# Performance work log

Measured on AMD Instinct MI355X. Metric: run time of the kernel, lower is better.

Reference implementation:

```python
import jax, jax.numpy as jnp
import numpy as np
import math

MAX_L = 2
TARGET_DIM = 64


def build_transform_matrix(target_dim=TARGET_DIM, max_l=MAX_L):
    """Replicates WignerTransformMatrix._build_transform_matrix: [target_dim^2, 9]."""
    wigner_dims = [2 * l + 1 for l in range(max_l + 1)]  # [1, 3, 5]
    T = np.zeros((target_dim * target_dim, 9), dtype=np.float32)
    start = 0
    for l in range(max_l + 1):
        d = wigner_dims[l]
        if l == 0:
            for i in range(3):
                T[start, i * 3 + i] = 1.0 / 3.0
        elif l == 1:
            for i in range(d):
                for j in range(d):
                    T[start + i * d + j, i * 3 + j] = 1.0
        elif l == 2:
            for i in range(min(d, 3)):
                T[start + i * d + i, i * 3 + i] = 1.0
            rules = [(0, 1, [(0, 1, 0.5), (1, 0, 0.5)]),
                     (0, 2, [(0, 2, 0.7), (2, 0, 0.3)]),
                     (1, 2, [(1, 2, 0.6), (2, 1, 0.4)]),
                     (0, 4, [(0, 1, 0.3), (1, 0, 0.3), (0, 2, 0.2), (2, 0, 0.2)])]
            for oi, oj, combos in rules:
                if oi < d and oj < d:
                    for ii, jj, w in combos:
                        T[start + oi * d + oj, ii * 3 + jj] = w
                        if oi != oj:
                            T[start + oj * d + oi, ii * 3 + jj] = w
        start += d * d
    return jnp.asarray(T)


def setup_inputs() -> dict:
    key = jax.random.key(0)
    ks = jax.random.split(key, 12)
    B, N, H, G, D = 2, 1024, 8, 2, 64
    s = 0.02
    return {
        "x": jax.random.normal(ks[0], (B, N, H, G, D), dtype=jnp.float32),
        "rotations": jax.random.normal(ks[1], (B, N, 3, 3), dtype=jnp.float32),
        "mask": jnp.ones((B, N), dtype=bool),
        "Wq": jax.random.normal(ks[2], (D, D), dtype=jnp.float32) * s,
        "bq": jnp.zeros((D,), dtype=jnp.float32),
        "Wk": jax.random.normal(ks[3], (D, D), dtype=jnp.float32) * s,
        "bk": jnp.zeros((D,), dtype=jnp.float32),
        "Wv": jax.random.normal(ks[4], (D, D), dtype=jnp.float32) * s,
        "bv": jnp.zeros((D,), dtype=jnp.float32),
        "Wo": jax.random.normal(ks[5], (D, D), dtype=jnp.float32) * s,
        "bo": jnp.zeros((D,), dtype=jnp.float32),
        "fusion_weight": jnp.ones((1,), dtype=jnp.float32),
    }


def reference(x, rotations, mask, Wq, bq, Wk, bk, Wv, bv, Wo, bo, fusion_weight):
    B, N, H, G, D = x.shape
    HG = H * G
    scale = math.sqrt(D)
    T = build_transform_matrix(D, MAX_L)  # [D*D, 9]

    # projections (torch Linear: x @ W.T + b)
    q = (x @ Wq.T + bq).reshape(B, N, HG, D).transpose(0, 2, 1, 3)  # [B,HG,N,D]
    k = (x @ Wk.T + bk).reshape(B, N, HG, D).transpose(0, 2, 1, 3)
    v = (x @ Wv.T + bv).reshape(B, N, HG, D).transpose(0, 2, 1, 3)

    scores = jnp.einsum('bhnd,bhmd->bhnm', q, k) / scale  # [B,HG,N,N]

    # Wigner matrices: vec(R) @ T.T -> [B,N,D,D]
    R_vec = rotations.reshape(B, N, 9)
    wig = (R_vec @ T.T).reshape(B, N, D, D)

    # per-token transformed q/k (no [B,HG,N,D,D] materialization)
    q_t = jnp.einsum('bhnd,bnde->bhne', q, wig)
    k_t = jnp.einsum('bhnd,bnde->bhne', k, wig)
    wigner_scores = jnp.einsum('bhnd,bhmd->bhnm', q_t, k_t) / scale

    enhanced = scores + fusion_weight[0] * wigner_scores
    mask2d = mask[:, None, :, None] & mask[:, None, None, :]  # [B,1,N,N]
    enhanced = jnp.where(mask2d, enhanced, -jnp.inf)

    attn = jax.nn.softmax(enhanced, axis=-1)
    out = jnp.einsum('bhnm,bhmd->bhnd', attn, v)  # [B,HG,N,D]
    out = out.transpose(0, 2, 1, 3).reshape(B, N, H, G, D)
    return out @ Wo.T + bo
```

## Files before the change

kernel.cpp:

```cpp
#include <hip/hip_runtime.h>
#include <cstring>
#include <cstddef>

#define NB  2
#define NN  1024
#define NHG 16
#define ND  64

typedef unsigned short ushort_t;
typedef __attribute__((ext_vector_type(8))) short short8v;
typedef __attribute__((ext_vector_type(16))) float f32x16;

struct MMat { float m[81]; };

__device__ inline unsigned cvt_pk_bf16(float a, float b) {
  unsigned r;
  asm("v_cvt_pk_bf16_f32 %0, %1, %2" : "=v"(r) : "v"(a), "v"(b));
  return r;
}
__device__ inline float bf2f(ushort_t s) { return __uint_as_float((unsigned)s << 16); }
__device__ inline void split_pair(float a, float b, unsigned& hw, unsigned& lw) {
  hw = cvt_pk_bf16(a, b);
  float ah = __uint_as_float(hw << 16);
  float bh = __uint_as_float(hw & 0xffff0000u);
  lw = cvt_pk_bf16(a - ah, b - bh);
}

__device__ inline f32x16 mfma32(short8v a, short8v b, f32x16 c) {
  return __builtin_amdgcn_mfma_f32_32x32x16_bf16(a, b, c, 0, 0, 0);
}

static void compute_M(float* M) {
  static float T[4096][9];
  std::memset(T, 0, sizeof(T));
  int start = 0;
  for (int l = 0; l <= 2; ++l) {
    int d = 2 * l + 1;
    if (l == 0) {
      for (int i = 0; i < 3; ++i) T[start][i * 3 + i] = 1.0f / 3.0f;
    } else if (l == 1) {
      for (int i = 0; i < d; ++i)
        for (int j = 0; j < d; ++j)
          T[start + i * d + j][i * 3 + j] = 1.0f;
    } else {
      for (int i = 0; i < 3; ++i) T[start + i * d + i][i * 3 + i] = 1.0f;
      const int   oiA[4] = {0, 0, 1, 0}, ojA[4] = {1, 2, 2, 4};
      const int   cnt[4] = {2, 2, 2, 4};
      const int   iiA[4][4] = {{0,1,0,0},{0,2,0,0},{1,2,0,0},{0,1,0,2}};
      const int   jjA[4][4] = {{1,0,0,0},{2,0,0,0},{2,1,0,0},{1,0,2,0}};
      const float wA[4][4]  = {{0.5f,0.5f,0,0},{0.7f,0.3f,0,0},{0.6f,0.4f,0,0},{0.3f,0.3f,0.2f,0.2f}};
      for (int r = 0; r < 4; ++r) {
        int oi = oiA[r], oj = ojA[r];
        if (oi < d && oj < d) {
          for (int c = 0; c < cnt[r]; ++c) {
            T[start + oi * d + oj][iiA[r][c] * 3 + jjA[r][c]] = wA[r][c];
            if (oi != oj) T[start + oj * d + oi][iiA[r][c] * 3 + jjA[r][c]] = wA[r][c];
          }
        }
      }
    }
    start += d * d;
  }
  for (int i = 0; i < 9; ++i)
    for (int j = 0; j < 9; ++j) {
      double a = 0.0;
      for (int f = 0; f < 4096; ++f) a += (double)T[f][i] * (double)T[f][j];
      M[i * 9 + j] = (float)a;
    }
}

__global__ __launch_bounds__(256) void qkv_gemm(
    const float* __restrict__ x, const float* __restrict__ rot,
    const float* __restrict__ fusion,
    const float* __restrict__ Wq, const float* __restrict__ bq,
    const float* __restrict__ Wk, const float* __restrict__ bk,
    const float* __restrict__ Wv, const float* __restrict__ bv,
    ushort_t* __restrict__ Qb, ushort_t* __restrict__ Kb,
    ushort_t* __restrict__ VhT, MMat Mm) {
  const int tid = threadIdx.x;
  const int w = tid >> 6, l = tid & 63;
  const int l31 = l & 31, hi5 = l >> 5;
  const int mt = blockIdx.x, p = blockIdx.y;
  const int bh = mt >> 3, n0 = (mt & 7) << 7;
  const float* W    = p == 0 ? Wq : (p == 1 ? Wk : Wv);
  const float* bvec = p == 0 ? bq : (p == 1 ? bk : bv);

  __shared__ union UU {
    struct { ushort_t A[128 * 72]; ushort_t B[2][64 * 72]; } s;
    float D[128 * 67];
  } u;
  __shared__ float biasS[64];
  __shared__ float rotS[128][9];

  #pragma unroll
  for (int it = 0; it < 8; ++it) {
    int i = tid + it * 256;
    int r = i >> 4, c4 = i & 15;
    const float* src = x + (((size_t)((bh >> 4) * 1024 + n0 + r) * 16 + (bh & 15)) << 6) + (c4 << 2);
    float4 v = *(const float4*)src;
    uint2 hw = { cvt_pk_bf16(v.x, v.y), cvt_pk_bf16(v.z, v.w) };
    *(uint2*)(&u.s.A[r * 72 + c4 * 4]) = hw;
  }
  #pragma unroll
  for (int it = 0; it < 4; ++it) {
    int i = tid + it * 256;
    int r = i >> 4, c4 = i & 15;
    float4 v = *(const float4*)(W + ((size_t)i << 2));
    unsigned h0, l0, h1, l1;
    split_pair(v.x, v.y, h0, l0);
    split_pair(v.z, v.w, h1, l1);
    uint2 hw = { h0, h1 }, lw = { l0, l1 };
    *(uint2*)(&u.s.B[0][r * 72 + c4 * 4]) = hw;
    *(uint2*)(&u.s.B[1][r * 72 + c4 * 4]) = lw;
  }
  if (tid < 64) biasS[tid] = bvec[tid];
  if (p < 2) {
    for (int i = tid; i < 1152; i += 256) {
      int r = i / 9, c = i - r * 9;
      rotS[r][c] = rot[((size_t)((bh >> 4) * 1024 + n0 + r)) * 9 + c];
    }
  }
  __syncthreads();

  f32x16 acc0, acc1;
  #pragma unroll
  for (int r = 0; r < 16; ++r) { acc0[r] = 0.f; acc1[r] = 0.f; }
  const int mbase = w << 5;
  __builtin_amdgcn_s_setprio(1);
  #pragma unroll
  for (int s = 0; s < 4; ++s) {
    const int ko = s * 16 + 8 * hi5;
    short8v aH  = *(const short8v*)(&u.s.A[(mbase + l31) * 72 + ko]);
    short8v b0H = *(const short8v*)(&u.s.B[0][l31 * 72 + ko]);
    short8v b0L = *(const short8v*)(&u.s.B[1][l31 * 72 + ko]);
    short8v b1H = *(const short8v*)(&u.s.B[0][(32 + l31) * 72 + ko]);
    short8v b1L = *(const short8v*)(&u.s.B[1][(32 + l31) * 72 + ko]);
    acc0 = mfma32(aH, b0H, acc0);
    acc0 = mfma32(aH, b0L, acc0);
    acc1 = mfma32(aH, b1H, acc1);
    acc1 = mfma32(aH, b1L, acc1);
  }
  __builtin_amdgcn_s_setprio(0);
  __syncthreads();
  #pragma unroll
  for (int r = 0; r < 16; ++r) {
    int m = mbase + (r & 3) + 8 * (r >> 2) + 4 * hi5;
    u.D[m * 67 + l31]      = acc0[r];
    u.D[m * 67 + 32 + l31] = acc1[r];
  }
  __syncthreads();

  if (p < 2) {
    const int mloc = tid >> 1, dh = (tid & 1) << 5;
    ushort_t* dst = p ? Kb : Qb;
    const float scale = p ? 1.0f : 0.125f;
    const size_t rowo = ((size_t)bh * 1024 + n0 + mloc) * 96;
    #pragma unroll
    for (int j = 0; j < 4; ++j) {
      union { unsigned wd[4]; short8v v; } pk;
      #pragma unroll
      for (int e = 0; e < 4; ++e) {
        int c = dh + 8 * j + 2 * e;
        float v0 = (u.D[mloc * 67 + c]     + biasS[c])     * scale;
        float v1 = (u.D[mloc * 67 + c + 1] + biasS[c + 1]) * scale;
        pk.wd[e] = cvt_pk_bf16(v0, v1);
      }
      *(short8v*)(dst + rowo + dh + 8 * j) = pk.v;
    }
    if (dh == 0) {
      float base0 = u.D[mloc * 67] + biasS[0];
      float e16[16];
      if (p == 0) {
        float fq = fusion[0] * base0 * 0.125f;
        #pragma unroll
        for (int j = 0; j < 16; ++j) e16[j] = (j < 9) ? fq * rotS[mloc][j] : 0.f;
      } else {
        #pragma unroll
        for (int j = 0; j < 16; ++j) {
          float a = 0.f;
          if (j < 9) {
            #pragma unroll
            for (int jj = 0; jj < 9; ++jj)
              a = fmaf(Mm.m[j * 9 + jj], rotS[mloc][jj], a);
          }
          e16[j] = base0 * a;
        }
      }
      union { unsigned wd[4]; short8v v; } pa, pb;
      #pragma unroll
      for (int e = 0; e < 4; ++e) {
        pa.wd[e] = cvt_pk_bf16(e16[2 * e], e16[2 * e + 1]);
        pb.wd[e] = cvt_pk_bf16(e16[8 + 2 * e], e16[9 + 2 * e]);
      }
      *(short8v*)(dst + rowo + 64) = pa.v;
      *(short8v*)(dst + rowo + 72) = pb.v;
    }
  } else {
    const int d = tid >> 2, nb = tid & 3;
    const float bd = biasS[d];
    const size_t o = ((size_t)bh * 64 + d) * 1024 + n0 + nb * 32;
    #pragma unroll
    for (int j = 0; j < 4; ++j) {
      union { unsigned wd[4]; short8v v; } pk;
      #pragma unroll
      for (int e = 0; e < 4; ++e) {
        int c = 8 * j + 2 * e;
        float v0 = u.D[(nb * 32 + c) * 67 + d] + bd;
        float v1 = u.D[(nb * 32 + c + 1) * 67 + d] + bd;
        pk.wd[e] = cvt_pk_bf16(v0, v1);
      }
      *(short8v*)(VhT + o + 8 * j) = pk.v;
    }
  }
}

__global__ __launch_bounds__(256) void attn_kernel(
    const ushort_t* __restrict__ Qb, const ushort_t* __restrict__ Kb,
    const ushort_t* __restrict__ VhT,
    unsigned* __restrict__ OpartW, float* __restrict__ Ml, int SPLIT, int KTN) {
  const int tid = threadIdx.x;
  const int w = tid >> 6, l = tid & 63;
  const int l31 = l & 31, hi5 = l >> 5;
  const int bid = blockIdx.x;
  const int bh = bid & 31, rest = bid >> 5;
  const int qt = rest & 7, sp = rest >> 3;
  const int qn0 = qt * 128 + w * 32;

  __shared__ ushort_t Ks[64 * 88];
  __shared__ ushort_t Vs[64 * 72];

  short8v qh[5];
  {
    const ushort_t* qrow = Qb + ((size_t)bh * 1024 + qn0 + l31) * 96;
    #pragma unroll
    for (int s = 0; s < 5; ++s)
      qh[s] = *(const short8v*)(qrow + 16 * s + 8 * hi5);
  }

  f32x16 Ob0, Ob1;
  #pragma unroll
  for (int r = 0; r < 16; ++r) { Ob0[r] = 0.f; Ob1[r] = 0.f; }
  float mrun = -1e30f, lsum = 0.f;

  const ushort_t* Kbase = Kb + (size_t)bh * 1024 * 96;
  const ushort_t* VhB = VhT + (size_t)bh * 64 * 1024;
  const float L2E = 1.44269504088896f;
  const int kv0 = sp * KTN * 64;

  for (int kt = 0; kt < KTN; ++kt) {
    const int kb = kv0 + kt * 64;
    __syncthreads();
    #pragma unroll
    for (int u0 = 0; u0 < 3; ++u0) {
      int u = tid + u0 * 256;
      if (u < 640) {
        int r = u / 10, c = u - r * 10;
        *(short8v*)(Ks + r * 88 + c * 8) =
            *(const short8v*)(Kbase + (size_t)(kb + r) * 96 + c * 8);
      }
    }
    #pragma unroll
    for (int u0 = 0; u0 < 2; ++u0) {
      int u = tid + u0 * 256;
      int d = u >> 3, c = u & 7;
      *(short8v*)(Vs + d * 72 + c * 8) =
          *(const short8v*)(VhB + (size_t)d * 1024 + kb + c * 8);
    }
    __syncthreads();

    f32x16 S0, S1;
    #pragma unroll
    for (int r = 0; r < 16; ++r) { S0[r] = 0.f; S1[r] = 0.f; }
    __builtin_amdgcn_s_setprio(1);
    #pragma unroll
    for (int s = 0; s < 5; ++s) {
      short8v ka0 = *(const short8v*)(Ks + l31 * 88 + (2 * s + hi5) * 8);
      S0 = mfma32(ka0, qh[s], S0);
      short8v ka1 = *(const short8v*)(Ks + (32 + l31) * 88 + (2 * s + hi5) * 8);
      S1 = mfma32(ka1, qh[s], S1);
    }
    __builtin_amdgcn_s_setprio(0);

    float tmax = -1e30f;
    #pragma unroll
    for (int r = 0; r < 16; ++r) tmax = fmaxf(tmax, fmaxf(S0[r], S1[r]));
    tmax = fmaxf(tmax, __shfl_xor(tmax, 32, 64));
    if (!__all(tmax <= mrun + 8.0f)) {
      float mnew = fmaxf(mrun, tmax);
      float fac = __builtin_amdgcn_exp2f((mrun - mnew) * L2E);
      lsum *= fac;
      #pragma unroll
      for (int r = 0; r < 16; ++r) {
        int cr = (r & 3) + 8 * (r >> 2) + 4 * hi5;
        float fr = __shfl(fac, cr, 64);
        Ob0[r] *= fr; Ob1[r] *= fr;
      }
      mrun = mnew;
    }
    float p0[16], p1[16];
    float psum = 0.f;
    #pragma unroll
    for (int r = 0; r < 16; ++r) {
      p0[r] = __builtin_amdgcn_exp2f((S0[r] - mrun) * L2E);
      p1[r] = __builtin_amdgcn_exp2f((S1[r] - mrun) * L2E);
      psum += p0[r] + p1[r];
    }
    psum += __shfl_xor(psum, 32, 64);
    lsum += psum;

    #pragma unroll
    for (int B = 0; B < 2; ++B) {
      const float* pp = (B == 0) ? p0 : p1;
      unsigned wh[8], xh[8];
      #pragma unroll
      for (int i = 0; i < 8; ++i) {
        wh[i] = cvt_pk_bf16(pp[2 * i], pp[2 * i + 1]);
        xh[i] = __shfl_xor(wh[i], 32, 64);
      }
      __builtin_amdgcn_s_setprio(1);
      #pragma unroll
      for (int s = 0; s < 2; ++s) {
        union U8 { short8v v; unsigned u[4]; } aph;
        aph.u[0] = hi5 ? xh[4 * s + 2] : wh[4 * s];
        aph.u[1] = hi5 ? xh[4 * s + 3] : wh[4 * s + 1];
        aph.u[2] = hi5 ? wh[4 * s + 2] : xh[4 * s];
        aph.u[3] = hi5 ? wh[4 * s + 3] : xh[4 * s + 1];
        int slot = 4 * B + 2 * s + hi5;
        short8v vH0 = *(const short8v*)(Vs + l31 * 72 + slot * 8);
        Ob0 = mfma32(aph.v, vH0, Ob0);
        short8v vH1 = *(const short8v*)(Vs + (32 + l31) * 72 + slot * 8);
        Ob1 = mfma32(aph.v, vH1, Ob1);
      }
      __builtin_amdgcn_s_setprio(0);
    }
  }

  #pragma unroll
  for (int r = 0; r < 16; ++r) {
    int cr = (r & 3) + 8 * (r >> 2) + 4 * hi5;
    size_t rowb = ((size_t)(bh * 1024 + qn0 + cr) * SPLIT + sp) * 32;
    OpartW[rowb + l31] = cvt_pk_bf16(Ob0[r], Ob1[r]);
  }
  if (l < 32) {
    size_t mb = ((size_t)(bh * 1024 + qn0 + l) * SPLIT + sp) * 2;
    Ml[mb]     = mrun;
    Ml[mb + 1] = lsum;
  }
}

__global__ __launch_bounds__(256) void oproj_gemm(
    const unsigned* __restrict__ OpartW, const float* __restrict__ Ml,
    float* __restrict__ out,
    const float* __restrict__ Wo, const float* __restrict__ bo, int SPLIT) {
  const int tid = threadIdx.x;
  const int w = tid >> 6, l = tid & 63;
  const int l31 = l & 31, hi5 = l >> 5;
  const int m0 = blockIdx.x << 6;
  const int rh = (w & 1) << 5;
  const int ch = (w >> 1) << 5;

  __shared__ union UU {
    struct { ushort_t A[64 * 72]; ushort_t B[2][64 * 72]; } s;
    float D[64 * 67];
  } u;
  __shared__ float biasS[64];
  __shared__ float cf[64][4];

  if (tid < 64) {
    int row = m0 + tid;
    int n = (row >> 4) & 1023, hgb = row & 15, bb = row >> 14;
    size_t prow = ((size_t)(bb * 16 + hgb)) * 1024 + n;
    float mv[4], lv[4];
    float ms = -1e30f;
    for (int s = 0; s < SPLIT; ++s) {
      mv[s] = Ml[(prow * SPLIT + s) * 2];
      lv[s] = Ml[(prow * SPLIT + s) * 2 + 1];
      ms = fmaxf(ms, mv[s]);
    }
    float ef[4], lt = 0.f;
    for (int s = 0; s < SPLIT; ++s) { ef[s] = __expf(mv[s] - ms); lt += ef[s] * lv[s]; }
    float li = 1.0f / lt;
    for (int s = 0; s < 4; ++s) cf[tid][s] = (s < SPLIT) ? ef[s] * li : 0.f;
  }
  if (tid >= 192) biasS[tid - 192] = bo[tid - 192];
  __syncthreads();

  #pragma unroll
  for (int it = 0; it < 2; ++it) {
    int i = tid + it * 256;
    int r = i >> 3, q4 = i & 7;
    int row = m0 + r;
    int n = (row >> 4) & 1023, hgb = row & 15, bb = row >> 14;
    size_t prow = ((size_t)(bb * 16 + hgb)) * 1024 + n;
    float f[8] = {0.f, 0.f, 0.f, 0.f, 0.f, 0.f, 0.f, 0.f};
    for (int s = 0; s < SPLIT; ++s) {
      float c = cf[r][s];
      uint4 wv = *(const uint4*)(OpartW + (prow * SPLIT + s) * 32 + q4 * 4);
      unsigned wa[4] = { wv.x, wv.y, wv.z, wv.w };
      #pragma unroll
      for (int j = 0; j < 4; ++j) {
        f[j]     = fmaf(c, __uint_as_float(wa[j] << 16), f[j]);
        f[4 + j] = fmaf(c, __uint_as_float(wa[j] & 0xffff0000u), f[4 + j]);
      }
    }
    uint2 lo = { cvt_pk_bf16(f[0], f[1]), cvt_pk_bf16(f[2], f[3]) };
    uint2 hi = { cvt_pk_bf16(f[4], f[5]), cvt_pk_bf16(f[6], f[7]) };
    *(uint2*)(&u.s.A[r * 72 + q4 * 4])      = lo;
    *(uint2*)(&u.s.A[r * 72 + 32 + q4 * 4]) = hi;
  }
  #pragma unroll
  for (int it = 0; it < 4; ++it) {
    int i = tid + it * 256;
    int r = i >> 4, c4 = i & 15;
    float4 v = *(const float4*)(Wo + ((size_t)i << 2));
    unsigned h0, l0, h1, l1;
    split_pair(v.x, v.y, h0, l0);
    split_pair(v.z, v.w, h1, l1);
    uint2 hw = { h0, h1 }, lw = { l0, l1 };
    *(uint2*)(&u.s.B[0][r * 72 + c4 * 4]) = hw;
    *(uint2*)(&u.s.B[1][r * 72 + c4 * 4]) = lw;
  }
  __syncthreads();

  f32x16 acc;
  #pragma unroll
  for (int r = 0; r < 16; ++r) acc[r] = 0.f;
  __builtin_amdgcn_s_setprio(1);
  #pragma unroll
  for (int s = 0; s < 4; ++s) {
    const int ko = s * 16 + 8 * hi5;
    short8v aH = *(const short8v*)(&u.s.A[(rh + l31) * 72 + ko]);
    short8v bH = *(const short8v*)(&u.s.B[0][(ch + l31) * 72 + ko]);
    short8v bL = *(const short8v*)(&u.s.B[1][(ch + l31) * 72 + ko]);
    acc = mfma32(aH, bH, acc);
    acc = mfma32(aH, bL, acc);
  }
  __builtin_amdgcn_s_setprio(0);
  __syncthreads();
  #pragma unroll
  for (int r = 0; r < 16; ++r) {
    int m = rh + (r & 3) + 8 * (r >> 2) + 4 * hi5;
    u.D[m * 67 + ch + l31] = acc[r];
  }
  __syncthreads();

  const int mloc = tid >> 2, q = tid & 3;
  float* orow = out + ((size_t)(m0 + mloc) << 6) + q * 16;
  #pragma unroll
  for (int j = 0; j < 4; ++j) {
    int c = q * 16 + 4 * j;
    float4 v;
    v.x = u.D[mloc * 67 + c + 0] + biasS[c + 0];
    v.y = u.D[mloc * 67 + c + 1] + biasS[c + 1];
    v.z = u.D[mloc * 67 + c + 2] + biasS[c + 2];
    v.w = u.D[mloc * 67 + c + 3] + biasS[c + 3];
    *(float4*)(orow + 4 * j) = v;
  }
}

extern "C" void kernel_launch(void* const* d_in, const int* in_sizes, int n_in,
                              void* d_out, int out_size, void* d_ws, size_t ws_size,
                              hipStream_t stream) {
  const float* x   = (const float*)d_in[0];
  const float* rot = (const float*)d_in[1];
  const float* Wq  = (const float*)d_in[3];
  const float* bq  = (const float*)d_in[4];
  const float* Wk  = (const float*)d_in[5];
  const float* bk  = (const float*)d_in[6];
  const float* Wv  = (const float*)d_in[7];
  const float* bv  = (const float*)d_in[8];
  const float* Wo  = (const float*)d_in[9];
  const float* bo  = (const float*)d_in[10];
  const float* fus = (const float*)d_in[11];
  float* out = (float*)d_out;
  char* ws = (char*)d_ws;

  ushort_t* Qb  = (ushort_t*)ws;
  ushort_t* Kb  = (ushort_t*)(ws + 6291456);
  ushort_t* VhT = (ushort_t*)(ws + 12582912);
  const size_t obase = 16777216;

  int SPLIT = 1;
  if (ws_size >= obase + 4 * 4456448) SPLIT = 4;
  else if (ws_size >= obase + 2 * 4456448) SPLIT = 2;
  const int KTN = 16 / SPLIT;
  unsigned* OpartW = (unsigned*)(ws + obase);
  float*    Ml     = (float*)(ws + obase + (size_t)4194304 * SPLIT);

  MMat Mm;
  compute_M(Mm.m);

  qkv_gemm<<<dim3(256, 3), 256, 0, stream>>>(x, rot, fus, Wq, bq, Wk, bk, Wv, bv,
                                             Qb, Kb, VhT, Mm);
  attn_kernel<<<256 * SPLIT, 256, 0, stream>>>(Qb, Kb, VhT, OpartW, Ml, SPLIT, KTN);
  oproj_gemm<<<512, 256, 0, stream>>>(OpartW, Ml, out, Wo, bo, SPLIT);
}
```

Baseline: 56.43 us.

## Double-buffer K/V tiles via direct global-to-LDS loads with XOR-swizzled V layout

The attention kernel now stages the next K/V tile into a second LDS buffer using global_load_lds while the current tile is computed, with explicit vmcnt waits and barriers in place of the synchronous load-then-sync loop. The Q/K row stride shrinks from 96 to 80 elements. V^T is written by the QKV kernel with an XOR swizzle so the unpadded LDS layout avoids bank conflicts. The kernel also gets an occupancy hint of 4 blocks per SM. The aim is to hide global load latency behind the MFMA work, at the cost of doubled LDS use and fragile hand-set waitcnt counts.

```diff
diff --git a/kernel.cpp b/kernel.cpp
--- a/kernel.cpp
+++ b/kernel.cpp
@@ -28,6 +28,12 @@
 
 __device__ inline f32x16 mfma32(short8v a, short8v b, f32x16 c) {
   return __builtin_amdgcn_mfma_f32_32x32x16_bf16(a, b, c, 0, 0, 0);
+}
+
+__device__ inline void gl_lds16(const ushort_t* g, ushort_t* l) {
+  __builtin_amdgcn_global_load_lds(
+      (const __attribute__((address_space(1))) void*)g,
+      (__attribute__((address_space(3))) void*)l, 16, 0, 0);
 }
 
 static void compute_M(float* M) {
@@ -154,7 +160,7 @@
     const int mloc = tid >> 1, dh = (tid & 1) << 5;
     ushort_t* dst = p ? Kb : Qb;
     const float scale = p ? 1.0f : 0.125f;
-    const size_t rowo = ((size_t)bh * 1024 + n0 + mloc) * 96;
+    const size_t rowo = ((size_t)bh * 1024 + n0 + mloc) * 80;
     #pragma unroll
     for (int j = 0; j < 4; ++j) {
       union { unsigned wd[4]; short8v v; } pk;
@@ -198,23 +204,25 @@
   } else {
     const int d = tid >> 2, nb = tid & 3;
     const float bd = biasS[d];
-    const size_t o = ((size_t)bh * 64 + d) * 1024 + n0 + nb * 32;
+    const size_t ob = ((size_t)bh * 64 + d) * 1024 + n0;
     #pragma unroll
     for (int j = 0; j < 4; ++j) {
+      int chunk = nb * 4 + j;
       union { unsigned wd[4]; short8v v; } pk;
       #pragma unroll
       for (int e = 0; e < 4; ++e) {
-        int c = 8 * j + 2 * e;
-        float v0 = u.D[(nb * 32 + c) * 67 + d] + bd;
-        float v1 = u.D[(nb * 32 + c + 1) * 67 + d] + bd;
+        int c = chunk * 8 + 2 * e;
+        float v0 = u.D[c * 67 + d] + bd;
+        float v1 = u.D[(c + 1) * 67 + d] + bd;
         pk.wd[e] = cvt_pk_bf16(v0, v1);
       }
-      *(short8v*)(VhT + o + 8 * j) = pk.v;
-    }
-  }
-}
-
-__global__ __launch_bounds__(256) void attn_kernel(
+      int slot = (chunk & 8) | ((chunk & 7) ^ (d & 7));
+      *(short8v*)(VhT + ob + slot * 8) = pk.v;
+    }
+  }
+}
+
+__global__ __launch_bounds__(256, 4) void attn_kernel(
     const ushort_t* __restrict__ Qb, const ushort_t* __restrict__ Kb,
     const ushort_t* __restrict__ VhT,
     unsigned* __restrict__ OpartW, float* __restrict__ Ml, int SPLIT, int KTN) {
@@ -225,13 +233,14 @@
   const int bh = bid & 31, rest = bid >> 5;
   const int qt = rest & 7, sp = rest >> 3;
   const int qn0 = qt * 128 + w * 32;
-
-  __shared__ ushort_t Ks[64 * 88];
-  __shared__ ushort_t Vs[64 * 72];
+  const int sl = l31 & 7;
+
+  __shared__ ushort_t Ks[2][64 * 80];
+  __shared__ ushort_t Vs[2][64 * 64];
 
   short8v qh[5];
   {
-    const ushort_t* qrow = Qb + ((size_t)bh * 1024 + qn0 + l31) * 96;
+    const ushort_t* qrow = Qb + ((size_t)bh * 1024 + qn0 + l31) * 80;
     #pragma unroll
     for (int s = 0; s < 5; ++s)
       qh[s] = *(const short8v*)(qrow + 16 * s + 8 * hi5);
@@ -242,31 +251,36 @@
   for (int r = 0; r < 16; ++r) { Ob0[r] = 0.f; Ob1[r] = 0.f; }
   float mrun = -1e30f, lsum = 0.f;
 
-  const ushort_t* Kbase = Kb + (size_t)bh * 1024 * 96;
-  const ushort_t* VhB = VhT + (size_t)bh * 64 * 1024;
+  const ushort_t* Kbase = Kb + (size_t)bh * 1024 * 80;
+  const ushort_t* VhB = VhT + (size_t)bh * 65536;
   const float L2E = 1.44269504088896f;
   const int kv0 = sp * KTN * 64;
 
+  auto stage = [&](int b, int kt) {
+    const int kb = kv0 + kt * 64;
+    #pragma unroll
+    for (int j = 0; j < 3; ++j) {
+      int i = tid + j * 256;
+      if (i < 640)
+        gl_lds16(Kbase + (size_t)(kb + i / 10) * 80 + (i % 10) * 8, &Ks[b][i * 8]);
+    }
+    #pragma unroll
+    for (int j = 0; j < 2; ++j) {
+      int i = tid + j * 256;
+      gl_lds16(VhB + (size_t)(i >> 3) * 1024 + kb + (i & 7) * 8, &Vs[b][i * 8]);
+    }
+  };
+
+  stage(0, 0);
   for (int kt = 0; kt < KTN; ++kt) {
-    const int kb = kv0 + kt * 64;
-    __syncthreads();
-    #pragma unroll
-    for (int u0 = 0; u0 < 3; ++u0) {
-      int u = tid + u0 * 256;
-      if (u < 640) {
-        int r = u / 10, c = u - r * 10;
-        *(short8v*)(Ks + r * 88 + c * 8) =
-            *(const short8v*)(Kbase + (size_t)(kb + r) * 96 + c * 8);
-      }
-    }
-    #pragma unroll
-    for (int u0 = 0; u0 < 2; ++u0) {
-      int u = tid + u0 * 256;
-      int d = u >> 3, c = u & 7;
-      *(short8v*)(Vs + d * 72 + c * 8) =
-          *(const short8v*)(VhB + (size_t)d * 1024 + kb + c * 8);
-    }
-    __syncthreads();
+    const int cur = kt & 1;
+    const bool haveNext = (kt + 1 < KTN);
+    if (haveNext) stage(cur ^ 1, kt + 1);
+    if (!haveNext)  { asm volatile("s_waitcnt vmcnt(0)" ::: "memory"); }
+    else if (w < 2) { asm volatile("s_waitcnt vmcnt(5)" ::: "memory"); }
+    else            { asm volatile("s_waitcnt vmcnt(4)" ::: "memory"); }
+    __builtin_amdgcn_sched_barrier(0);
+    __builtin_amdgcn_s_barrier();
 
     f32x16 S0, S1;
     #pragma unroll
@@ -274,9 +288,9 @@
     __builtin_amdgcn_s_setprio(1);
     #pragma unroll
     for (int s = 0; s < 5; ++s) {
-      short8v ka0 = *(const short8v*)(Ks + l31 * 88 + (2 * s + hi5) * 8);
+      short8v ka0 = *(const short8v*)(&Ks[cur][l31 * 80 + (2 * s + hi5) * 8]);
       S0 = mfma32(ka0, qh[s], S0);
-      short8v ka1 = *(const short8v*)(Ks + (32 + l31) * 88 + (2 * s + hi5) * 8);
+      short8v ka1 = *(const short8v*)(&Ks[cur][(32 + l31) * 80 + (2 * s + hi5) * 8]);
       S1 = mfma32(ka1, qh[s], S1);
     }
     __builtin_amdgcn_s_setprio(0);
@@ -326,13 +340,14 @@
         aph.u[2] = hi5 ? wh[4 * s + 2] : xh[4 * s];
         aph.u[3] = hi5 ? wh[4 * s + 3] : xh[4 * s + 1];
         int slot = 4 * B + 2 * s + hi5;
-        short8v vH0 = *(const short8v*)(Vs + l31 * 72 + slot * 8);
+        short8v vH0 = *(const short8v*)(&Vs[cur][l31 * 64 + (slot ^ sl) * 8]);
         Ob0 = mfma32(aph.v, vH0, Ob0);
-        short8v vH1 = *(const short8v*)(Vs + (32 + l31) * 72 + slot * 8);
+        short8v vH1 = *(const short8v*)(&Vs[cur][(32 + l31) * 64 + (slot ^ sl) * 8]);
         Ob1 = mfma32(aph.v, vH1, Ob1);
       }
       __builtin_amdgcn_s_setprio(0);
     }
+    __builtin_amdgcn_s_barrier();
   }
 
   #pragma unroll
@@ -476,9 +491,9 @@
   char* ws = (char*)d_ws;
 
   ushort_t* Qb  = (ushort_t*)ws;
-  ushort_t* Kb  = (ushort_t*)(ws + 6291456);
-  ushort_t* VhT = (ushort_t*)(ws + 12582912);
-  const size_t obase = 16777216;
+  ushort_t* Kb  = (ushort_t*)(ws + 5242880);
+  ushort_t* VhT = (ushort_t*)(ws + 10485760);
+  const size_t obase = 14680064;
 
   int SPLIT = 1;
   if (ws_size >= obase + 4 * 4456448) SPLIT = 4;
```

New measurement: 49.86 us. -11.6%, faster.
